# Performance work log

Measured on AMD Instinct MI355X. Metric: run time of the kernel, lower is better.

Reference implementation:

```python
import jax, jax.numpy as jnp
import numpy as np

HEADS = 4
DIM_HEAD = 32
EPS = 1e-5


def setup_inputs() -> dict:
    key = jax.random.key(0)
    ks = jax.random.split(key, 3)
    B, H, W, C = 16, 64, 64, 128
    hidden = HEADS * DIM_HEAD  # 128
    x = jax.random.normal(ks[0], (B, H, W, C), dtype=jnp.float32)
    w_qkv = jax.random.normal(ks[1], (C, 3 * hidden), dtype=jnp.float32) * 0.05
    w_out = jax.random.normal(ks[2], (hidden, C), dtype=jnp.float32) * 0.05
    b_out = jnp.zeros((C,), dtype=jnp.float32)
    g_ln = jnp.ones((C,), dtype=jnp.float32)
    b_ln = jnp.zeros((C,), dtype=jnp.float32)
    return {"x": x, "w_qkv": w_qkv, "w_out": w_out, "b_out": b_out,
            "g_ln": g_ln, "b_ln": b_ln}


def reference(x, w_qkv, w_out, b_out, g_ln, b_ln):
    B, H, W, C = x.shape
    scale = DIM_HEAD ** -0.5
    n = H * W
    # 1x1 conv == channel matmul: [B,H,W,C] @ [C,3*hidden]
    qkv = jnp.einsum('bhwc,cf->bhwf', x, w_qkv)
    q, k, v = jnp.split(qkv, 3, axis=-1)
    # rearrange 'b x y (h c) -> b h c (x y)'
    def to_heads(t):
        return t.reshape(B, n, HEADS, DIM_HEAD).transpose(0, 2, 3, 1)  # [B,h,d,n]
    q, k, v = map(to_heads, (q, k, v))
    q = jax.nn.softmax(q, axis=-2) * scale   # softmax over channel dim d
    k = jax.nn.softmax(k, axis=-1)           # softmax over spatial dim n
    context = jnp.einsum('bhdn,bhen->bhde', k, v)  # [B,h,d,e] small
    out = jnp.einsum('bhde,bhdn->bhen', context, q)  # [B,h,e,n]
    # rearrange 'b h c (x y) -> b x y (h c)'
    out = out.transpose(0, 3, 1, 2).reshape(B, H, W, HEADS * DIM_HEAD)
    # to_out: 1x1 conv with bias, then LayerNorm over last dim
    out = jnp.einsum('bhwc,cd->bhwd', out, w_out) + b_out
    mean = jnp.mean(out, axis=-1, keepdims=True)
    var = jnp.var(out, axis=-1, keepdims=True)
    out = (out - mean) / jnp.sqrt(var + EPS) * g_ln + b_ln
    return out
```

## Files before the change

kernel.cpp:

```cpp
#include <hip/hip_runtime.h>
#include <hip/hip_bf16.h>
#include <cstddef>
#include <cstdint>


typedef __attribute__((ext_vector_type(8))) short short8_t;
typedef __attribute__((ext_vector_type(4))) float f32x4;

#define SCALE_Q 0.17677669529663687f
#define EPS_LN 1e-5f

__device__ __forceinline__ unsigned short f2bf(float f) {
  union { float f; unsigned u; } v; v.f = f;
  unsigned r = (v.u + 0x7FFFu + ((v.u >> 16) & 1u)) >> 16;
  return (unsigned short)r;
}
__device__ __forceinline__ float bf2f(unsigned short u) {
  union { float f; unsigned u; } v; v.u = ((unsigned)u) << 16;
  return v.f;
}

__device__ __forceinline__ short8_t trunc8(float4 lo, float4 hi) {
  union { float4 f; unsigned u[4]; } a, b;
  union { unsigned u[4]; short8_t s; } r;
  a.f = lo; b.f = hi;
  r.u[0] = __builtin_amdgcn_perm(a.u[1], a.u[0], 0x07060302);
  r.u[1] = __builtin_amdgcn_perm(a.u[3], a.u[2], 0x07060302);
  r.u[2] = __builtin_amdgcn_perm(b.u[1], b.u[0], 0x07060302);
  r.u[3] = __builtin_amdgcn_perm(b.u[3], b.u[2], 0x07060302);
  return r.s;
}

__global__ void k_transpose_wqkv(const float* __restrict__ w,
                                 unsigned short* __restrict__ wT) {
  int c = blockIdx.x * 4 + (threadIdx.x >> 6);
  int l = threadIdx.x & 63;
  float f0 = w[(size_t)(2 * l) * 384 + c];
  float f1 = w[(size_t)(2 * l + 1) * 384 + c];
  unsigned p = (unsigned)f2bf(f0) | ((unsigned)f2bf(f1) << 16);
  ((unsigned*)(wT + (size_t)c * 128))[l] = p;
}

__global__ __launch_bounds__(256, 4)
void k_q_soft(const float* __restrict__ x, const unsigned short* __restrict__ wT,
              unsigned short* __restrict__ qs) {
  __shared__ short Bq[128][136];
  int tid = threadIdx.x;
  int rowBase = blockIdx.x * 64;

  {
#pragma unroll
    for (int i = 0; i < 8; ++i) {
      int idx = i * 256 + tid;
      int n = idx >> 4;
      int k8 = (idx & 15) << 3;
      *(short8_t*)&Bq[n][k8] = *(const short8_t*)(wT + (size_t)n * 128 + k8);
    }
  }

  int lane = tid & 63;
  int wv = tid >> 6;
  int wr = wv >> 1, wc = wv & 1;
  int lr = lane & 15;
  int kg = lane >> 4;

  short8_t abf[4][2];
  {
    const float* ap = x + (size_t)(rowBase + wr * 32 + lr) * 128 + kg * 8;
#pragma unroll
    for (int mf = 0; mf < 2; ++mf) {
      const float* r = ap + (size_t)mf * 16 * 128;
#pragma unroll
      for (int kk = 0; kk < 4; ++kk)
        abf[kk][mf] = trunc8(*(const float4*)(r + kk * 32),
                             *(const float4*)(r + kk * 32 + 4));
    }
  }
  __syncthreads();

  f32x4 acc[2][4] = {};
#pragma unroll
  for (int kk = 0; kk < 4; ++kk) {
    short8_t bf[4];
#pragma unroll
    for (int nf = 0; nf < 4; ++nf)
      bf[nf] = *(const short8_t*)&Bq[wc * 64 + nf * 16 + lr][kk * 32 + kg * 8];
#pragma unroll
    for (int mf = 0; mf < 2; ++mf)
#pragma unroll
      for (int nf = 0; nf < 4; ++nf)
        acc[mf][nf] = __builtin_amdgcn_mfma_f32_16x16x32_bf16(abf[kk][mf], bf[nf], acc[mf][nf], 0, 0, 0);
  }

#pragma unroll
  for (int hg = 0; hg < 2; ++hg) {
#pragma unroll
    for (int mf = 0; mf < 2; ++mf) {
#pragma unroll
      for (int j = 0; j < 4; ++j) {
        float e0 = __expf(acc[mf][hg * 2][j]);
        float e1 = __expf(acc[mf][hg * 2 + 1][j]);
        float s = e0 + e1;
#pragma unroll
        for (int d = 1; d < 16; d <<= 1) s += __shfl_xor(s, d, 64);
        float inv = SCALE_Q / s;
        int tok = rowBase + wr * 32 + mf * 16 + kg * 4 + j;
        int hd = wc * 64 + hg * 32 + lr;
        qs[(size_t)tok * 128 + hd] = f2bf(e0 * inv);
        qs[(size_t)tok * 128 + hd + 16] = f2bf(e1 * inv);
      }
    }
  }
}

__global__ __launch_bounds__(256, 2)
void k_kv_ctx(const float* __restrict__ x, const unsigned short* __restrict__ wT,
              float* __restrict__ ctxp, float* __restrict__ ksump) {
  __shared__ short Bk[128][136];
  __shared__ short Bv[128][136];

  int tid = threadIdx.x;
  int rb = blockIdx.x;
  int rowBase = rb * 128;

  {
    const unsigned short* wk = wT + (size_t)1 * 128 * 128;
    const unsigned short* wv2 = wT + (size_t)2 * 128 * 128;
#pragma unroll
    for (int i = 0; i < 8; ++i) {
      int idx = i * 256 + tid;
      int n = idx >> 4;
      int k8 = (idx & 15) << 3;
      *(short8_t*)&Bk[n][k8] = *(const short8_t*)(wk + (size_t)n * 128 + k8);
      *(short8_t*)&Bv[n][k8] = *(const short8_t*)(wv2 + (size_t)n * 128 + k8);
    }
  }

  int lane = tid & 63;
  int wv = tid >> 6;
  int wr = wv >> 1, wc = wv & 1;
  int lr = lane & 15;
  int kg = lane >> 4;

  short8_t abf[4][4];
  {
    const float* ap = x + (size_t)(rowBase + wr * 64 + lr) * 128 + kg * 8;
#pragma unroll
    for (int mf = 0; mf < 4; ++mf) {
      const float* r = ap + (size_t)mf * 16 * 128;
#pragma unroll
      for (int kk = 0; kk < 4; ++kk)
        abf[kk][mf] = trunc8(*(const float4*)(r + kk * 32),
                             *(const float4*)(r + kk * 32 + 4));
    }
  }
  __syncthreads();

  uint2 ekp[4][4], vp[4][4];
  {
    f32x4 acc[4][4] = {};
#pragma unroll
    for (int kk = 0; kk < 4; ++kk) {
      short8_t bf[4];
#pragma unroll
      for (int nf = 0; nf < 4; ++nf)
        bf[nf] = *(const short8_t*)&Bk[wc * 64 + nf * 16 + lr][kk * 32 + kg * 8];
#pragma unroll
      for (int mf = 0; mf < 4; ++mf)
#pragma unroll
        for (int nf = 0; nf < 4; ++nf)
          acc[mf][nf] = __builtin_amdgcn_mfma_f32_16x16x32_bf16(abf[kk][mf], bf[nf], acc[mf][nf], 0, 0, 0);
    }
#pragma unroll
    for (int mf = 0; mf < 4; ++mf)
#pragma unroll
      for (int nf = 0; nf < 4; ++nf) {
        unsigned s0 = f2bf(__expf(acc[mf][nf][0])), s1 = f2bf(__expf(acc[mf][nf][1]));
        unsigned s2 = f2bf(__expf(acc[mf][nf][2])), s3 = f2bf(__expf(acc[mf][nf][3]));
        ekp[mf][nf].x = s0 | (s1 << 16);
        ekp[mf][nf].y = s2 | (s3 << 16);
      }
  }
  {
    f32x4 acc[4][4] = {};
#pragma unroll
    for (int kk = 0; kk < 4; ++kk) {
      short8_t bf[4];
#pragma unroll
      for (int nf = 0; nf < 4; ++nf)
        bf[nf] = *(const short8_t*)&Bv[wc * 64 + nf * 16 + lr][kk * 32 + kg * 8];
#pragma unroll
      for (int mf = 0; mf < 4; ++mf)
#pragma unroll
        for (int nf = 0; nf < 4; ++nf)
          acc[mf][nf] = __builtin_amdgcn_mfma_f32_16x16x32_bf16(abf[kk][mf], bf[nf], acc[mf][nf], 0, 0, 0);
    }
#pragma unroll
    for (int mf = 0; mf < 4; ++mf)
#pragma unroll
      for (int nf = 0; nf < 4; ++nf) {
        unsigned s0 = f2bf(acc[mf][nf][0]), s1 = f2bf(acc[mf][nf][1]);
        unsigned s2 = f2bf(acc[mf][nf][2]), s3 = f2bf(acc[mf][nf][3]);
        vp[mf][nf].x = s0 | (s1 << 16);
        vp[mf][nf].y = s2 | (s3 << 16);
      }
  }
  __syncthreads();

  short (*ekT)[136] = Bk;
  short (*vT)[136] = Bv;
#pragma unroll
  for (int mf = 0; mf < 4; ++mf) {
    int t0 = wr * 64 + mf * 16 + kg * 4;
#pragma unroll
    for (int nf = 0; nf < 4; ++nf) {
      int col = wc * 64 + nf * 16 + lr;
      *(uint2*)&ekT[col][t0] = ekp[mf][nf];
      *(uint2*)&vT[col][t0] = vp[mf][nf];
    }
  }
  __syncthreads();

  {
    int h = wv;
    f32x4 c2[2][2] = {};
#pragma unroll
    for (int kk = 0; kk < 4; ++kk) {
      short8_t a2[2], b2[2];
#pragma unroll
      for (int m2 = 0; m2 < 2; ++m2)
        a2[m2] = *(const short8_t*)&ekT[h * 32 + m2 * 16 + lr][kk * 32 + kg * 8];
#pragma unroll
      for (int n2 = 0; n2 < 2; ++n2)
        b2[n2] = *(const short8_t*)&vT[h * 32 + n2 * 16 + lr][kk * 32 + kg * 8];
#pragma unroll
      for (int m2 = 0; m2 < 2; ++m2)
#pragma unroll
        for (int n2 = 0; n2 < 2; ++n2)
          c2[m2][n2] = __builtin_amdgcn_mfma_f32_16x16x32_bf16(a2[m2], b2[n2], c2[m2][n2], 0, 0, 0);
    }
    float* cp = ctxp + ((size_t)rb * 4 + h) * 1024;
#pragma unroll
    for (int m2 = 0; m2 < 2; ++m2)
#pragma unroll
      for (int n2 = 0; n2 < 2; ++n2)
#pragma unroll
        for (int j = 0; j < 4; ++j)
          cp[(m2 * 16 + kg * 4 + j) * 32 + n2 * 16 + lr] = c2[m2][n2][j];
  }

  if (tid < 128) {
    float s = 0;
#pragma unroll
    for (int t8 = 0; t8 < 128; t8 += 8) {
      short8_t v8 = *(const short8_t*)&ekT[tid][t8];
#pragma unroll
      for (int i = 0; i < 8; ++i) s += bf2f((unsigned short)v8[i]);
    }
    ksump[(size_t)rb * 128 + tid] = s;
  }
}

__global__ __launch_bounds__(256, 4)
void k_weff64(const float* __restrict__ ctxp, const float* __restrict__ ksump,
              const float* __restrict__ wout, unsigned short* __restrict__ weffT) {
  __shared__ float wo[32][128];
  __shared__ float cn[32][32];
  __shared__ float ksh[32];
  int tid = threadIdx.x;
  int b = blockIdx.x >> 2, h = blockIdx.x & 3;

#pragma unroll
  for (int i = 0; i < 16; ++i) {
    int idx = i * 256 + tid;
    int e = idx >> 7, jj = idx & 127;
    wo[e][jj] = wout[(h * 32 + e) * 128 + jj];
  }
  if (tid < 32) {
    float s = 0;
    for (int c = 0; c < 32; ++c)
      s += ksump[(size_t)(b * 32 + c) * 128 + h * 32 + tid];
    ksh[tid] = s;
  }
  __syncthreads();
#pragma unroll
  for (int i = 0; i < 4; ++i) {
    int idx = i * 256 + tid;
    int d = idx >> 5, e = idx & 31;
    float s = 0;
    for (int c = 0; c < 32; ++c)
      s += ctxp[((size_t)(b * 32 + c) * 4 + h) * 1024 + idx];
    cn[d][e] = s / ksh[d];
  }
  __syncthreads();

  int j = tid >> 1, dg = tid & 1;
  unsigned short acc16[16];
#pragma unroll
  for (int dd = 0; dd < 16; ++dd) {
    int d = dg * 16 + dd;
    float s = 0;
#pragma unroll
    for (int e = 0; e < 32; ++e) s += cn[d][e] * wo[e][j];
    acc16[dd] = f2bf(s);
  }
  unsigned short* outp = weffT + (size_t)b * 16384 + j * 128 + h * 32 + dg * 16;
  *(short8_t*)outp = *(short8_t*)&acc16[0];
  *(short8_t*)(outp + 8) = *(short8_t*)&acc16[8];
}

__global__ __launch_bounds__(256, 2)
void k_out_ln(const unsigned short* __restrict__ qs, const unsigned short* __restrict__ weffT,
              const float* __restrict__ b_out, const float* __restrict__ g_ln,
              const float* __restrict__ b_ln, float* __restrict__ out) {
  int tid = threadIdx.x;
  int rowBase = blockIdx.x * 128;
  int b = rowBase >> 12;
  int lane = tid & 63;
  int w = tid >> 6;
  int lr = lane & 15;
  int kg = lane >> 4;

  const unsigned short* bb = weffT + (size_t)b * 16384;

  short8_t a[2][4];
  {
    const unsigned short* ap = qs + (size_t)(rowBase + w * 32 + lr) * 128 + kg * 8;
#pragma unroll
    for (int mf = 0; mf < 2; ++mf)
#pragma unroll
      for (int kk = 0; kk < 4; ++kk)
        a[mf][kk] = *(const short8_t*)(ap + (size_t)mf * 16 * 128 + kk * 32);
  }

  f32x4 acc[2][8] = {};
#pragma unroll
  for (int kk = 0; kk < 4; ++kk) {
    short8_t bf[8];
#pragma unroll
    for (int nf = 0; nf < 8; ++nf)
      bf[nf] = *(const short8_t*)(bb + (size_t)(nf * 16 + lr) * 128 + kk * 32 + kg * 8);
#pragma unroll
    for (int mf = 0; mf < 2; ++mf)
#pragma unroll
      for (int nf = 0; nf < 8; ++nf)
        acc[mf][nf] = __builtin_amdgcn_mfma_f32_16x16x32_bf16(a[mf][kk], bf[nf], acc[mf][nf], 0, 0, 0);
  }

  float bo[8], gl[8], bl[8];
#pragma unroll
  for (int nf = 0; nf < 8; ++nf) {
    int c = nf * 16 + lr;
    bo[nf] = b_out[c]; gl[nf] = g_ln[c]; bl[nf] = b_ln[c];
  }
#pragma unroll
  for (int mf = 0; mf < 2; ++mf)
#pragma unroll
    for (int nf = 0; nf < 8; ++nf)
#pragma unroll
      for (int j = 0; j < 4; ++j) acc[mf][nf][j] += bo[nf];

#pragma unroll
  for (int mf = 0; mf < 2; ++mf) {
    float s[4] = {0, 0, 0, 0}, q[4] = {0, 0, 0, 0};
#pragma unroll
    for (int nf = 0; nf < 8; ++nf)
#pragma unroll
      for (int j = 0; j < 4; ++j) {
        float v = acc[mf][nf][j];
        s[j] += v; q[j] += v * v;
      }
#pragma unroll
    for (int j = 0; j < 4; ++j) {
#pragma unroll
      for (int d = 1; d < 16; d <<= 1) {
        s[j] += __shfl_xor(s[j], d, 64);
        q[j] += __shfl_xor(q[j], d, 64);
      }
    }
#pragma unroll
    for (int j = 0; j < 4; ++j) {
      float mean = s[j] * (1.0f / 128.0f);
      float var = q[j] * (1.0f / 128.0f) - mean * mean;
      float rstd = rsqrtf(var + EPS_LN);
      size_t ro = (size_t)(rowBase + w * 32 + mf * 16 + kg * 4 + j) * 128;
#pragma unroll
      for (int nf = 0; nf < 8; ++nf)
        out[ro + nf * 16 + lr] = (acc[mf][nf][j] - mean) * rstd * gl[nf] + bl[nf];
    }
  }
}

extern "C" void kernel_launch(void* const* d_in, const int* in_sizes, int n_in,
                              void* d_out, int out_size, void* d_ws, size_t ws_size,
                              hipStream_t stream) {
  const float* x     = (const float*)d_in[0];
  const float* w_qkv = (const float*)d_in[1];
  const float* w_out = (const float*)d_in[2];
  const float* b_out = (const float*)d_in[3];
  const float* g_ln  = (const float*)d_in[4];
  const float* b_ln  = (const float*)d_in[5];
  float* out = (float*)d_out;

  char* ws = (char*)d_ws;
  unsigned short* wqkvT = (unsigned short*)(ws + 0);
  float* ctxp           = (float*)(ws + 131072);
  float* ksump          = (float*)(ws + 131072 + 8388608);
  unsigned short* weffT = (unsigned short*)(ws + 131072 + 8388608 + 262144);
  unsigned short* qs    = (unsigned short*)(ws + 131072 + 8388608 + 262144 + 524288);

  k_transpose_wqkv<<<96, 256, 0, stream>>>(w_qkv, wqkvT);
  k_q_soft<<<1024, 256, 0, stream>>>(x, wqkvT, qs);
  k_kv_ctx<<<512, 256, 0, stream>>>(x, wqkvT, ctxp, ksump);
  k_weff64<<<64, 256, 0, stream>>>(ctxp, ksump, w_out, weffT);
  k_out_ln<<<512, 256, 0, stream>>>(qs, weffT, b_out, g_ln, b_ln, out);
}
```

Baseline: 63.07 us.

## Fuse Q projection and softmax into output projection and LayerNorm kernel

Removes the separate Q-softmax kernel and its bf16 qs round trip through global memory. The final kernel now reloads x, computes Q^T with MFMA using the transposed weight as the A operand, and applies the channel softmax. It stages the normalized Q in shared memory and then runs the weff GEMM plus bias and LayerNorm. This saves one launch and a 16MB write/read, at the cost of reading x a second time in the last kernel and reading weight tiles straight from global memory instead of LDS.

```diff
diff --git a/kernel.cpp b/kernel.cpp
--- a/kernel.cpp
+++ b/kernel.cpp
@@ -30,6 +30,10 @@
   r.u[3] = __builtin_amdgcn_perm(b.u[3], b.u[2], 0x07060302);
   return r.s;
 }
+__device__ __forceinline__ unsigned pack2(float f0, float f1) {
+  union { float f; unsigned u; } a, b; a.f = f0; b.f = f1;
+  return __builtin_amdgcn_perm(b.u, a.u, 0x07060302);
+}
 
 __global__ void k_transpose_wqkv(const float* __restrict__ w,
                                  unsigned short* __restrict__ wT) {
@@ -41,78 +45,6 @@
   ((unsigned*)(wT + (size_t)c * 128))[l] = p;
 }
 
-__global__ __launch_bounds__(256, 4)
-void k_q_soft(const float* __restrict__ x, const unsigned short* __restrict__ wT,
-              unsigned short* __restrict__ qs) {
-  __shared__ short Bq[128][136];
-  int tid = threadIdx.x;
-  int rowBase = blockIdx.x * 64;
-
-  {
-#pragma unroll
-    for (int i = 0; i < 8; ++i) {
-      int idx = i * 256 + tid;
-      int n = idx >> 4;
-      int k8 = (idx & 15) << 3;
-      *(short8_t*)&Bq[n][k8] = *(const short8_t*)(wT + (size_t)n * 128 + k8);
-    }
-  }
-
-  int lane = tid & 63;
-  int wv = tid >> 6;
-  int wr = wv >> 1, wc = wv & 1;
-  int lr = lane & 15;
-  int kg = lane >> 4;
-
-  short8_t abf[4][2];
-  {
-    const float* ap = x + (size_t)(rowBase + wr * 32 + lr) * 128 + kg * 8;
-#pragma unroll
-    for (int mf = 0; mf < 2; ++mf) {
-      const float* r = ap + (size_t)mf * 16 * 128;
-#pragma unroll
-      for (int kk = 0; kk < 4; ++kk)
-        abf[kk][mf] = trunc8(*(const float4*)(r + kk * 32),
-                             *(const float4*)(r + kk * 32 + 4));
-    }
-  }
-  __syncthreads();
-
-  f32x4 acc[2][4] = {};
-#pragma unroll
-  for (int kk = 0; kk < 4; ++kk) {
-    short8_t bf[4];
-#pragma unroll
-    for (int nf = 0; nf < 4; ++nf)
-      bf[nf] = *(const short8_t*)&Bq[wc * 64 + nf * 16 + lr][kk * 32 + kg * 8];
-#pragma unroll
-    for (int mf = 0; mf < 2; ++mf)
-#pragma unroll
-      for (int nf = 0; nf < 4; ++nf)
-        acc[mf][nf] = __builtin_amdgcn_mfma_f32_16x16x32_bf16(abf[kk][mf], bf[nf], acc[mf][nf], 0, 0, 0);
-  }
-
-#pragma unroll
-  for (int hg = 0; hg < 2; ++hg) {
-#pragma unroll
-    for (int mf = 0; mf < 2; ++mf) {
-#pragma unroll
-      for (int j = 0; j < 4; ++j) {
-        float e0 = __expf(acc[mf][hg * 2][j]);
-        float e1 = __expf(acc[mf][hg * 2 + 1][j]);
-        float s = e0 + e1;
-#pragma unroll
-        for (int d = 1; d < 16; d <<= 1) s += __shfl_xor(s, d, 64);
-        float inv = SCALE_Q / s;
-        int tok = rowBase + wr * 32 + mf * 16 + kg * 4 + j;
-        int hd = wc * 64 + hg * 32 + lr;
-        qs[(size_t)tok * 128 + hd] = f2bf(e0 * inv);
-        qs[(size_t)tok * 128 + hd + 16] = f2bf(e1 * inv);
-      }
-    }
-  }
-}
-
 __global__ __launch_bounds__(256, 2)
 void k_kv_ctx(const float* __restrict__ x, const unsigned short* __restrict__ wT,
               float* __restrict__ ctxp, float* __restrict__ ksump) {
@@ -309,42 +241,76 @@
   *(short8_t*)(outp + 8) = *(short8_t*)&acc16[8];
 }
 
-__global__ __launch_bounds__(256, 2)
-void k_out_ln(const unsigned short* __restrict__ qs, const unsigned short* __restrict__ weffT,
-              const float* __restrict__ b_out, const float* __restrict__ g_ln,
-              const float* __restrict__ b_ln, float* __restrict__ out) {
+__global__ __launch_bounds__(256, 4)
+void k_qout2(const float* __restrict__ x, const unsigned short* __restrict__ wT,
+             const unsigned short* __restrict__ weffT,
+             const float* __restrict__ b_out, const float* __restrict__ g_ln,
+             const float* __restrict__ b_ln, float* __restrict__ out) {
+  __shared__ short QS[64][132];
+
   int tid = threadIdx.x;
-  int rowBase = blockIdx.x * 128;
-  int b = rowBase >> 12;
   int lane = tid & 63;
   int w = tid >> 6;
   int lr = lane & 15;
   int kg = lane >> 4;
-
-  const unsigned short* bb = weffT + (size_t)b * 16384;
-
-  short8_t a[2][4];
-  {
-    const unsigned short* ap = qs + (size_t)(rowBase + w * 32 + lr) * 128 + kg * 8;
-#pragma unroll
-    for (int mf = 0; mf < 2; ++mf)
-#pragma unroll
-      for (int kk = 0; kk < 4; ++kk)
-        a[mf][kk] = *(const short8_t*)(ap + (size_t)mf * 16 * 128 + kk * 32);
-  }
-
-  f32x4 acc[2][8] = {};
+  int tokBase = blockIdx.x * 64;
+  int b = blockIdx.x >> 6;
+  int myTok = tokBase + w * 16 + lr;
+
+  short8_t bx[4];
+  {
+    const float* xp = x + (size_t)myTok * 128 + kg * 8;
+#pragma unroll
+    for (int kk = 0; kk < 4; ++kk)
+      bx[kk] = trunc8(*(const float4*)(xp + kk * 32),
+                      *(const float4*)(xp + kk * 32 + 4));
+  }
+
+  f32x4 acc[8] = {};
 #pragma unroll
   for (int kk = 0; kk < 4; ++kk) {
-    short8_t bf[8];
-#pragma unroll
-    for (int nf = 0; nf < 8; ++nf)
-      bf[nf] = *(const short8_t*)(bb + (size_t)(nf * 16 + lr) * 128 + kk * 32 + kg * 8);
-#pragma unroll
-    for (int mf = 0; mf < 2; ++mf)
-#pragma unroll
-      for (int nf = 0; nf < 8; ++nf)
-        acc[mf][nf] = __builtin_amdgcn_mfma_f32_16x16x32_bf16(a[mf][kk], bf[nf], acc[mf][nf], 0, 0, 0);
+#pragma unroll
+    for (int mf = 0; mf < 8; ++mf) {
+      short8_t aq = *(const short8_t*)(wT + (size_t)(mf * 16 + lr) * 128 + kk * 32 + kg * 8);
+      acc[mf] = __builtin_amdgcn_mfma_f32_16x16x32_bf16(aq, bx[kk], acc[mf], 0, 0, 0);
+    }
+  }
+
+#pragma unroll
+  for (int h = 0; h < 4; ++h) {
+    float s = 0;
+#pragma unroll
+    for (int mh = 0; mh < 2; ++mh) {
+      int mf = 2 * h + mh;
+#pragma unroll
+      for (int j = 0; j < 4; ++j) {
+        acc[mf][j] = __expf(acc[mf][j]);
+        s += acc[mf][j];
+      }
+    }
+    s += __shfl_xor(s, 16, 64);
+    s += __shfl_xor(s, 32, 64);
+    float inv = SCALE_Q / s;
+#pragma unroll
+    for (int mh = 0; mh < 2; ++mh) {
+      int mf = 2 * h + mh;
+      uint2 p;
+      p.x = pack2(acc[mf][0] * inv, acc[mf][1] * inv);
+      p.y = pack2(acc[mf][2] * inv, acc[mf][3] * inv);
+      *(uint2*)&QS[w * 16 + lr][mf * 16 + kg * 4] = p;
+    }
+  }
+
+  const unsigned short* wb = weffT + (size_t)b * 16384;
+  f32x4 acc2[8] = {};
+#pragma unroll
+  for (int kk = 0; kk < 4; ++kk) {
+    short8_t aq2 = *(const short8_t*)&QS[w * 16 + lr][kk * 32 + kg * 8];
+#pragma unroll
+    for (int nf = 0; nf < 8; ++nf) {
+      short8_t bw = *(const short8_t*)(wb + (size_t)(nf * 16 + lr) * 128 + kk * 32 + kg * 8);
+      acc2[nf] = __builtin_amdgcn_mfma_f32_16x16x32_bf16(aq2, bw, acc2[nf], 0, 0, 0);
+    }
   }
 
   float bo[8], gl[8], bl[8];
@@ -354,40 +320,35 @@
     bo[nf] = b_out[c]; gl[nf] = g_ln[c]; bl[nf] = b_ln[c];
   }
 #pragma unroll
-  for (int mf = 0; mf < 2; ++mf)
+  for (int nf = 0; nf < 8; ++nf)
+#pragma unroll
+    for (int j = 0; j < 4; ++j) acc2[nf][j] += bo[nf];
+
+  float s[4] = {0, 0, 0, 0}, q[4] = {0, 0, 0, 0};
+#pragma unroll
+  for (int nf = 0; nf < 8; ++nf)
+#pragma unroll
+    for (int j = 0; j < 4; ++j) {
+      float v = acc2[nf][j];
+      s[j] += v; q[j] += v * v;
+    }
+#pragma unroll
+  for (int j = 0; j < 4; ++j) {
+#pragma unroll
+    for (int d = 1; d < 16; d <<= 1) {
+      s[j] += __shfl_xor(s[j], d, 64);
+      q[j] += __shfl_xor(q[j], d, 64);
+    }
+  }
+#pragma unroll
+  for (int j = 0; j < 4; ++j) {
+    float mean = s[j] * (1.0f / 128.0f);
+    float var = q[j] * (1.0f / 128.0f) - mean * mean;
+    float rstd = rsqrtf(var + EPS_LN);
+    size_t ro = (size_t)(tokBase + w * 16 + kg * 4 + j) * 128;
 #pragma unroll
     for (int nf = 0; nf < 8; ++nf)
-#pragma unroll
-      for (int j = 0; j < 4; ++j) acc[mf][nf][j] += bo[nf];
-
-#pragma unroll
-  for (int mf = 0; mf < 2; ++mf) {
-    float s[4] = {0, 0, 0, 0}, q[4] = {0, 0, 0, 0};
-#pragma unroll
-    for (int nf = 0; nf < 8; ++nf)
-#pragma unroll
-      for (int j = 0; j < 4; ++j) {
-        float v = acc[mf][nf][j];
-        s[j] += v; q[j] += v * v;
-      }
-#pragma unroll
-    for (int j = 0; j < 4; ++j) {
-#pragma unroll
-      for (int d = 1; d < 16; d <<= 1) {
-        s[j] += __shfl_xor(s[j], d, 64);
-        q[j] += __shfl_xor(q[j], d, 64);
-      }
-    }
-#pragma unroll
-    for (int j = 0; j < 4; ++j) {
-      float mean = s[j] * (1.0f / 128.0f);
-      float var = q[j] * (1.0f / 128.0f) - mean * mean;
-      float rstd = rsqrtf(var + EPS_LN);
-      size_t ro = (size_t)(rowBase + w * 32 + mf * 16 + kg * 4 + j) * 128;
-#pragma unroll
-      for (int nf = 0; nf < 8; ++nf)
-        out[ro + nf * 16 + lr] = (acc[mf][nf][j] - mean) * rstd * gl[nf] + bl[nf];
-    }
+      out[ro + nf * 16 + lr] = (acc2[nf][j] - mean) * rstd * gl[nf] + bl[nf];
   }
 }
 
@@ -407,11 +368,9 @@
   float* ctxp           = (float*)(ws + 131072);
   float* ksump          = (float*)(ws + 131072 + 8388608);
   unsigned short* weffT = (unsigned short*)(ws + 131072 + 8388608 + 262144);
-  unsigned short* qs    = (unsigned short*)(ws + 131072 + 8388608 + 262144 + 524288);
 
   k_transpose_wqkv<<<96, 256, 0, stream>>>(w_qkv, wqkvT);
-  k_q_soft<<<1024, 256, 0, stream>>>(x, wqkvT, qs);
   k_kv_ctx<<<512, 256, 0, stream>>>(x, wqkvT, ctxp, ksump);
   k_weff64<<<64, 256, 0, stream>>>(ctxp, ksump, w_out, weffT);
-  k_out_ln<<<512, 256, 0, stream>>>(qs, weffT, b_out, g_ln, b_ln, out);
-}
+  k_qout2<<<1024, 256, 0, stream>>>(x, wqkvT, weffT, b_out, g_ln, b_ln, out);
+}
```

New measurement: 70.70 us. 12.1% more time.

## Pre-convert x to bf16 once, fold key sums into MFMA, pack bf16 stores

Applied to the files above, without the earlier changes.

Adds a kernel that truncates x to bf16 once, so the Q and K/V projection kernels load bf16 tiles directly instead of converting fp32 on the fly. Key-softmax denominators are now computed by an extra MFMA against a ones vector, replacing a serial per-thread LDS reduction. The q and weff outputs are written as packed bf16 pairs, with the head-dim contraction order permuted consistently between qs and weffT. All float-to-bf16 conversions now truncate rather than round. The trade-off is an extra launch and an additional write and read of a 16 MB bf16 copy of x.

```diff
diff --git a/kernel.cpp b/kernel.cpp
--- a/kernel.cpp
+++ b/kernel.cpp
@@ -19,16 +19,9 @@
   union { float f; unsigned u; } v; v.u = ((unsigned)u) << 16;
   return v.f;
 }
-
-__device__ __forceinline__ short8_t trunc8(float4 lo, float4 hi) {
-  union { float4 f; unsigned u[4]; } a, b;
-  union { unsigned u[4]; short8_t s; } r;
-  a.f = lo; b.f = hi;
-  r.u[0] = __builtin_amdgcn_perm(a.u[1], a.u[0], 0x07060302);
-  r.u[1] = __builtin_amdgcn_perm(a.u[3], a.u[2], 0x07060302);
-  r.u[2] = __builtin_amdgcn_perm(b.u[1], b.u[0], 0x07060302);
-  r.u[3] = __builtin_amdgcn_perm(b.u[3], b.u[2], 0x07060302);
-  return r.s;
+__device__ __forceinline__ unsigned pack2(float f0, float f1) {
+  union { float f; unsigned u; } a, b; a.f = f0; b.f = f1;
+  return __builtin_amdgcn_perm(b.u, a.u, 0x07060302);
 }
 
 __global__ void k_transpose_wqkv(const float* __restrict__ w,
@@ -37,12 +30,27 @@
   int l = threadIdx.x & 63;
   float f0 = w[(size_t)(2 * l) * 384 + c];
   float f1 = w[(size_t)(2 * l + 1) * 384 + c];
-  unsigned p = (unsigned)f2bf(f0) | ((unsigned)f2bf(f1) << 16);
-  ((unsigned*)(wT + (size_t)c * 128))[l] = p;
+  ((unsigned*)(wT + (size_t)c * 128))[l] = pack2(f0, f1);
+}
+
+__global__ void k_xbf(const float* __restrict__ x, unsigned* __restrict__ xbf) {
+  const float4* x4 = (const float4*)x;
+  uint2* o = (uint2*)xbf;
+  int base = blockIdx.x * 1024 + threadIdx.x;
+  float4 v[4];
+#pragma unroll
+  for (int it = 0; it < 4; ++it) v[it] = x4[base + it * 256];
+#pragma unroll
+  for (int it = 0; it < 4; ++it) {
+    uint2 p;
+    p.x = pack2(v[it].x, v[it].y);
+    p.y = pack2(v[it].z, v[it].w);
+    o[base + it * 256] = p;
+  }
 }
 
 __global__ __launch_bounds__(256, 4)
-void k_q_soft(const float* __restrict__ x, const unsigned short* __restrict__ wT,
+void k_q_soft(const unsigned short* __restrict__ xbf, const unsigned short* __restrict__ wT,
               unsigned short* __restrict__ qs) {
   __shared__ short Bq[128][136];
   int tid = threadIdx.x;
@@ -66,15 +74,12 @@
 
   short8_t abf[4][2];
   {
-    const float* ap = x + (size_t)(rowBase + wr * 32 + lr) * 128 + kg * 8;
-#pragma unroll
-    for (int mf = 0; mf < 2; ++mf) {
-      const float* r = ap + (size_t)mf * 16 * 128;
+    const unsigned short* ap = xbf + (size_t)(rowBase + wr * 32 + lr) * 128 + kg * 8;
+#pragma unroll
+    for (int mf = 0; mf < 2; ++mf)
 #pragma unroll
       for (int kk = 0; kk < 4; ++kk)
-        abf[kk][mf] = trunc8(*(const float4*)(r + kk * 32),
-                             *(const float4*)(r + kk * 32 + 4));
-    }
+        abf[kk][mf] = *(const short8_t*)(ap + (size_t)mf * 16 * 128 + kk * 32);
   }
   __syncthreads();
 
@@ -105,16 +110,15 @@
         for (int d = 1; d < 16; d <<= 1) s += __shfl_xor(s, d, 64);
         float inv = SCALE_Q / s;
         int tok = rowBase + wr * 32 + mf * 16 + kg * 4 + j;
-        int hd = wc * 64 + hg * 32 + lr;
-        qs[(size_t)tok * 128 + hd] = f2bf(e0 * inv);
-        qs[(size_t)tok * 128 + hd + 16] = f2bf(e1 * inv);
+        *(unsigned*)&qs[(size_t)tok * 128 + wc * 64 + hg * 32 + 2 * lr] =
+            pack2(e0 * inv, e1 * inv);
       }
     }
   }
 }
 
 __global__ __launch_bounds__(256, 2)
-void k_kv_ctx(const float* __restrict__ x, const unsigned short* __restrict__ wT,
+void k_kv_ctx(const unsigned short* __restrict__ xbf, const unsigned short* __restrict__ wT,
               float* __restrict__ ctxp, float* __restrict__ ksump) {
   __shared__ short Bk[128][136];
   __shared__ short Bv[128][136];
@@ -144,15 +148,12 @@
 
   short8_t abf[4][4];
   {
-    const float* ap = x + (size_t)(rowBase + wr * 64 + lr) * 128 + kg * 8;
-#pragma unroll
-    for (int mf = 0; mf < 4; ++mf) {
-      const float* r = ap + (size_t)mf * 16 * 128;
+    const unsigned short* ap = xbf + (size_t)(rowBase + wr * 64 + lr) * 128 + kg * 8;
+#pragma unroll
+    for (int mf = 0; mf < 4; ++mf)
 #pragma unroll
       for (int kk = 0; kk < 4; ++kk)
-        abf[kk][mf] = trunc8(*(const float4*)(r + kk * 32),
-                             *(const float4*)(r + kk * 32 + 4));
-    }
+        abf[kk][mf] = *(const short8_t*)(ap + (size_t)mf * 16 * 128 + kk * 32);
   }
   __syncthreads();
 
@@ -175,10 +176,8 @@
     for (int mf = 0; mf < 4; ++mf)
 #pragma unroll
       for (int nf = 0; nf < 4; ++nf) {
-        unsigned s0 = f2bf(__expf(acc[mf][nf][0])), s1 = f2bf(__expf(acc[mf][nf][1]));
-        unsigned s2 = f2bf(__expf(acc[mf][nf][2])), s3 = f2bf(__expf(acc[mf][nf][3]));
-        ekp[mf][nf].x = s0 | (s1 << 16);
-        ekp[mf][nf].y = s2 | (s3 << 16);
+        ekp[mf][nf].x = pack2(__expf(acc[mf][nf][0]), __expf(acc[mf][nf][1]));
+        ekp[mf][nf].y = pack2(__expf(acc[mf][nf][2]), __expf(acc[mf][nf][3]));
       }
   }
   {
@@ -199,10 +198,8 @@
     for (int mf = 0; mf < 4; ++mf)
 #pragma unroll
       for (int nf = 0; nf < 4; ++nf) {
-        unsigned s0 = f2bf(acc[mf][nf][0]), s1 = f2bf(acc[mf][nf][1]);
-        unsigned s2 = f2bf(acc[mf][nf][2]), s3 = f2bf(acc[mf][nf][3]);
-        vp[mf][nf].x = s0 | (s1 << 16);
-        vp[mf][nf].y = s2 | (s3 << 16);
+        vp[mf][nf].x = pack2(acc[mf][nf][0], acc[mf][nf][1]);
+        vp[mf][nf].y = pack2(acc[mf][nf][2], acc[mf][nf][3]);
       }
   }
   __syncthreads();
@@ -223,7 +220,12 @@
 
   {
     int h = wv;
+    union { unsigned u[4]; short8_t s; } ones;
+#pragma unroll
+    for (int i = 0; i < 4; ++i) ones.u[i] = 0x3F803F80u;
+
     f32x4 c2[2][2] = {};
+    f32x4 ks2[2] = {};
 #pragma unroll
     for (int kk = 0; kk < 4; ++kk) {
       short8_t a2[2], b2[2];
@@ -234,10 +236,12 @@
       for (int n2 = 0; n2 < 2; ++n2)
         b2[n2] = *(const short8_t*)&vT[h * 32 + n2 * 16 + lr][kk * 32 + kg * 8];
 #pragma unroll
-      for (int m2 = 0; m2 < 2; ++m2)
+      for (int m2 = 0; m2 < 2; ++m2) {
 #pragma unroll
         for (int n2 = 0; n2 < 2; ++n2)
           c2[m2][n2] = __builtin_amdgcn_mfma_f32_16x16x32_bf16(a2[m2], b2[n2], c2[m2][n2], 0, 0, 0);
+        ks2[m2] = __builtin_amdgcn_mfma_f32_16x16x32_bf16(a2[m2], ones.s, ks2[m2], 0, 0, 0);
+      }
     }
     float* cp = ctxp + ((size_t)rb * 4 + h) * 1024;
 #pragma unroll
@@ -247,17 +251,13 @@
 #pragma unroll
         for (int j = 0; j < 4; ++j)
           cp[(m2 * 16 + kg * 4 + j) * 32 + n2 * 16 + lr] = c2[m2][n2][j];
-  }
-
-  if (tid < 128) {
-    float s = 0;
-#pragma unroll
-    for (int t8 = 0; t8 < 128; t8 += 8) {
-      short8_t v8 = *(const short8_t*)&ekT[tid][t8];
-#pragma unroll
-      for (int i = 0; i < 8; ++i) s += bf2f((unsigned short)v8[i]);
-    }
-    ksump[(size_t)rb * 128 + tid] = s;
+    if (lr == 0) {
+#pragma unroll
+      for (int m2 = 0; m2 < 2; ++m2)
+#pragma unroll
+        for (int j = 0; j < 4; ++j)
+          ksump[(size_t)rb * 128 + h * 32 + m2 * 16 + kg * 4 + j] = ks2[m2][j];
+    }
   }
 }
 
@@ -286,27 +286,31 @@
 #pragma unroll
   for (int i = 0; i < 4; ++i) {
     int idx = i * 256 + tid;
-    int d = idx >> 5, e = idx & 31;
+    int d = idx >> 5;
     float s = 0;
     for (int c = 0; c < 32; ++c)
       s += ctxp[((size_t)(b * 32 + c) * 4 + h) * 1024 + idx];
-    cn[d][e] = s / ksh[d];
-  }
-  __syncthreads();
-
-  int j = tid >> 1, dg = tid & 1;
-  unsigned short acc16[16];
-#pragma unroll
-  for (int dd = 0; dd < 16; ++dd) {
-    int d = dg * 16 + dd;
-    float s = 0;
-#pragma unroll
-    for (int e = 0; e < 32; ++e) s += cn[d][e] * wo[e][j];
-    acc16[dd] = f2bf(s);
-  }
-  unsigned short* outp = weffT + (size_t)b * 16384 + j * 128 + h * 32 + dg * 16;
-  *(short8_t*)outp = *(short8_t*)&acc16[0];
-  *(short8_t*)(outp + 8) = *(short8_t*)&acc16[8];
+    cn[d][idx & 31] = s / ksh[d];
+  }
+  __syncthreads();
+
+  int j = tid >> 1, h8 = (tid & 1) * 8;
+  unsigned pk[8];
+#pragma unroll
+  for (int t = 0; t < 8; ++t) {
+    int dd = h8 + t;
+    float s0 = 0, s1 = 0;
+#pragma unroll
+    for (int e = 0; e < 32; ++e) {
+      float w = wo[e][j];
+      s0 += cn[dd][e] * w;
+      s1 += cn[16 + dd][e] * w;
+    }
+    pk[t] = pack2(s0, s1);
+  }
+  unsigned* outp = (unsigned*)(weffT + (size_t)b * 16384 + j * 128 + h * 32 + 2 * h8);
+  *(uint4*)outp = make_uint4(pk[0], pk[1], pk[2], pk[3]);
+  *(uint4*)(outp + 4) = make_uint4(pk[4], pk[5], pk[6], pk[7]);
 }
 
 __global__ __launch_bounds__(256, 2)
@@ -404,14 +408,16 @@
 
   char* ws = (char*)d_ws;
   unsigned short* wqkvT = (unsigned short*)(ws + 0);
-  float* ctxp           = (float*)(ws + 131072);
-  float* ksump          = (float*)(ws + 131072 + 8388608);
-  unsigned short* weffT = (unsigned short*)(ws + 131072 + 8388608 + 262144);
-  unsigned short* qs    = (unsigned short*)(ws + 131072 + 8388608 + 262144 + 524288);
+  unsigned short* xbf   = (unsigned short*)(ws + 131072);
+  float* ctxp           = (float*)(ws + 16908288);
+  float* ksump          = (float*)(ws + 25296896);
+  unsigned short* weffT = (unsigned short*)(ws + 25559040);
+  unsigned short* qs    = (unsigned short*)(ws + 26083328);
 
   k_transpose_wqkv<<<96, 256, 0, stream>>>(w_qkv, wqkvT);
-  k_q_soft<<<1024, 256, 0, stream>>>(x, wqkvT, qs);
-  k_kv_ctx<<<512, 256, 0, stream>>>(x, wqkvT, ctxp, ksump);
+  k_xbf<<<2048, 256, 0, stream>>>(x, (unsigned*)xbf);
+  k_q_soft<<<1024, 256, 0, stream>>>(xbf, wqkvT, qs);
+  k_kv_ctx<<<512, 256, 0, stream>>>(xbf, wqkvT, ctxp, ksump);
   k_weff64<<<64, 256, 0, stream>>>(ctxp, ksump, w_out, weffT);
   k_out_ln<<<512, 256, 0, stream>>>(qs, weffT, b_out, g_ln, b_ln, out);
 }
```

Result: slower. 79.83 us (+26.6%).
